# Kernel optimization log

Hardware: AMD Instinct MI355X
Metric: run time of the kernel (lower is better)

The kernel has to match this reference:

```python
import jax, jax.numpy as jnp
import numpy as np

N = 100_000   # nodes
E = 3_200_000 # edges (avg degree 32)
K = 10        # propagation hops


def setup_inputs() -> dict:
    key = jax.random.key(0)
    ks = jax.random.split(key, 9)
    x = jax.random.normal(ks[0], (N, 1), dtype=jnp.float32)
    edge_index = jax.random.randint(ks[1], (2, E), 0, N, dtype=jnp.int32)
    # MLP params (lin1: 1->32, lin2: 32->64, fc2: 64->1)
    W1 = jax.random.normal(ks[2], (1, 32), dtype=jnp.float32) * 0.5
    b1 = jnp.zeros((32,), dtype=jnp.float32)
    W2 = jax.random.normal(ks[3], (32, 64), dtype=jnp.float32) * (1.0 / np.sqrt(32))
    b2 = jnp.zeros((64,), dtype=jnp.float32)
    # GPR temp coefficients, Init='Random': uniform(-b, b), b=sqrt(3/(K+1)), L1-normalized
    bound = float(np.sqrt(3.0 / (K + 1)))
    temp = jax.random.uniform(ks[4], (K + 1,), dtype=jnp.float32,
                              minval=-bound, maxval=bound)
    temp = temp / jnp.sum(jnp.abs(temp))
    W_fc = jax.random.normal(ks[5], (64, 1), dtype=jnp.float32) * (1.0 / np.sqrt(64))
    b_fc = jnp.zeros((1,), dtype=jnp.float32)
    return {"x": x, "edge_index": edge_index, "W1": W1, "b1": b1,
            "W2": W2, "b2": b2, "temp": temp, "W_fc": W_fc, "b_fc": b_fc}


def reference(x, edge_index, W1, b1, W2, b2, temp, W_fc, b_fc):
    n = x.shape[0]
    # feature MLP
    h = jax.nn.relu(x @ W1 + b1)       # [N, 32]
    h = jax.nn.relu(h @ W2 + b2)       # [N, 64]
    # gcn_norm with self-loops, edge_weight = 1
    loops = jnp.arange(n, dtype=edge_index.dtype)
    row = jnp.concatenate([edge_index[0], loops])  # source
    col = jnp.concatenate([edge_index[1], loops])  # target (aggregation index)
    ones = jnp.ones(row.shape, dtype=h.dtype)
    deg = jax.ops.segment_sum(ones, col, num_segments=n)
    dinv = jnp.where(deg > 0, jax.lax.rsqrt(deg), 0.0)
    norm = dinv[row] * dinv[col]       # [E+N]
    # K-hop GPR propagation: hidden = sum_k temp[k] * A_hat^k h
    hidden0 = temp[0] * h

    def step(carry, gamma):
        xc, hid = carry
        msg = norm[:, None] * xc[row]                       # gather + scale
        xn = jax.ops.segment_sum(msg, col, num_segments=n)  # scatter-add
        return (xn, hid + gamma * xn), None

    (_, hidden), _ = jax.lax.scan(step, (h, hidden0), temp[1:])
    return hidden @ W_fc + b_fc        # [N, 1]
```

## Files before the change

kernel.cpp:

```cpp
#include <hip/hip_runtime.h>


#define TPB  256
#define SBSH 10
#define CAP1 34304
#define EPT  16
#define CH   (TPB * EPT)

__global__ void k_zero(int* __restrict__ bcursor, int nsb) {
    int i = blockIdx.x * blockDim.x + threadIdx.x;
    if (i < nsb) bcursor[i] = 0;
}

__global__ void k_scatter(const int* __restrict__ erow, const int* __restrict__ ecol,
                          int* __restrict__ bcursor, unsigned int* __restrict__ ebuf1,
                          int e, int nsb) {
    __shared__ int hist[128];
    __shared__ int base[128];
    int t = threadIdx.x;
    int s = blockIdx.x * CH;
    int r[EPT], c[EPT];

    if (t < 128) hist[t] = 0;
    __syncthreads();
#pragma unroll
    for (int j = 0; j < EPT; j++) {
        int i = s + j * TPB + t;
        bool ok = (i < e);
        c[j] = ok ? ecol[i] : -1;
        r[j] = ok ? erow[i] : 0;
        if (ok) atomicAdd(&hist[c[j] >> SBSH], 1);
    }
    __syncthreads();
    if (t < nsb) {
        int cc = hist[t];
        base[t] = cc ? atomicAdd(&bcursor[t], cc) : 0;
        hist[t] = 0;
    }
    __syncthreads();
#pragma unroll
    for (int j = 0; j < EPT; j++) {
        if (c[j] >= 0) {
            int b = c[j] >> SBSH;
            int pos = base[b] + atomicAdd(&hist[b], 1);
            if (pos < CAP1)
                ebuf1[(size_t)b * CAP1 + pos] =
                    ((unsigned int)r[j] << SBSH) | (unsigned int)(c[j] & ((1 << SBSH) - 1));
        }
    }
}

__global__ void __launch_bounds__(1024)
k_sub(const int* __restrict__ bcursor, const unsigned int* __restrict__ ebuf1,
      unsigned int* __restrict__ csr, int* __restrict__ rs, int* __restrict__ re,
      float* __restrict__ dinv, float* __restrict__ dinv2,
      float* __restrict__ sdeg, int n) {
    __shared__ int hist[1024];
    __shared__ int wsum[16];
    int b = blockIdx.x;
    int t = threadIdx.x;
    int lane = t & 63;
    int w = t >> 6;

    hist[t] = 0;
    __syncthreads();
    int cnt = min(bcursor[b], CAP1);
    size_t g = (size_t)b * CAP1;
    for (int j = t; j < cnt; j += 1024)
        atomicAdd(&hist[ebuf1[g + j] & 1023], 1);
    __syncthreads();

    int deg = hist[t];
    int v = deg;
#pragma unroll
    for (int o = 1; o < 64; o <<= 1) {
        int u = __shfl_up(v, o);
        if (lane >= o) v += u;
    }
    if (lane == 63) wsum[w] = v;
    __syncthreads();
    if (w == 0) {
        int sv = (lane < 16) ? wsum[lane] : 0;
#pragma unroll
        for (int o = 1; o < 16; o <<= 1) {
            int u = __shfl_up(sv, o);
            if (lane >= o) sv += u;
        }
        if (lane < 16) wsum[lane] = sv;
    }
    __syncthreads();
    int excl = v - deg + (w > 0 ? wsum[w - 1] : 0);

    int node = (b << SBSH) + t;
    if (node < n) {
        int base = (int)g + excl;
        rs[node] = base;
        re[node] = base + deg;
        float d = (float)(deg + 1);
        float di = rsqrtf(d);
        dinv[node] = di;
        dinv2[node] = di * di;
        sdeg[node] = d * di;
    }
    __syncthreads();
    hist[t] = excl;
    __syncthreads();
    for (int j = t; j < cnt; j += 1024) {
        unsigned int p = ebuf1[g + j];
        int sub = p & 1023;
        int pos = atomicAdd(&hist[sub], 1);
        csr[g + pos] = p >> SBSH;
    }
}

__global__ void k_mlp_z(const float* __restrict__ x, const float* __restrict__ W1,
                        const float* __restrict__ b1, const float* __restrict__ W2,
                        const float* __restrict__ b2, const float* __restrict__ Wfc,
                        const float* __restrict__ bfc, const float* __restrict__ temp,
                        const float* __restrict__ dinv,
                        float* __restrict__ u0, float* __restrict__ out, int n) {
    int wid = (blockIdx.x * blockDim.x + threadIdx.x) >> 6;
    int lane = threadIdx.x & 63;
    if (wid >= n) return;
    float xv = x[wid];
    float acc = b2[lane];
#pragma unroll
    for (int j = 0; j < 32; j++) {
        float h1 = fmaxf(fmaf(xv, W1[j], b1[j]), 0.f);
        acc = fmaf(h1, W2[j * 64 + lane], acc);
    }
    float h2 = fmaxf(acc, 0.f);
    float c = h2 * Wfc[lane];
#pragma unroll
    for (int o = 32; o >= 1; o >>= 1) c += __shfl_xor(c, o);
    if (lane == 0) {
        u0[wid] = dinv[wid] * c;
        out[wid] = fmaf(temp[0], c, bfc[0]);
    }
}

__global__ void k_hop(const int* __restrict__ rs, const int* __restrict__ re,
                      const unsigned int* __restrict__ csr,
                      const float* __restrict__ dinv2, const float* __restrict__ sdeg,
                      const float* __restrict__ uprev, float* __restrict__ ucur,
                      float* __restrict__ out, const float* __restrict__ temp,
                      int k, int n) {
    int tid = blockIdx.x * blockDim.x + threadIdx.x;
    int node = tid >> 3;
    int sub = tid & 7;
    if (node >= n) return;
    int s = rs[node];
    int epos = re[node];
    float sum = (sub == 0) ? uprev[node] : 0.f;
    for (int i = s + sub; i < epos; i += 8)
        sum += uprev[csr[i]];
    sum += __shfl_xor(sum, 1);
    sum += __shfl_xor(sum, 2);
    sum += __shfl_xor(sum, 4);
    if (sub == 0) {
        float u = dinv2[node] * sum;
        ucur[node] = u;
        out[node] = fmaf(temp[k] * sdeg[node], u, out[node]);
    }
}

static inline size_t align256(size_t x) { return (x + 255) & ~(size_t)255; }

extern "C" void kernel_launch(void* const* d_in, const int* in_sizes, int n_in,
                              void* d_out, int out_size, void* d_ws, size_t ws_size,
                              hipStream_t stream) {
    const float* x    = (const float*)d_in[0];
    const int*   ei   = (const int*)d_in[1];
    const float* W1   = (const float*)d_in[2];
    const float* b1   = (const float*)d_in[3];
    const float* W2   = (const float*)d_in[4];
    const float* b2   = (const float*)d_in[5];
    const float* temp = (const float*)d_in[6];
    const float* Wfc  = (const float*)d_in[7];
    const float* bfc  = (const float*)d_in[8];

    const int n = in_sizes[0];
    const int e = in_sizes[1] / 2;
    const int K = in_sizes[6] - 1;
    const int nsb = (n + (1 << SBSH) - 1) >> SBSH;

    const int* erow = ei;
    const int* ecol = ei + e;

    float* out = (float*)d_out;

    char* ws = (char*)d_ws;
    int*          bcursor = (int*)ws;          ws += align256((size_t)128 * 4);
    unsigned int* ebuf1   = (unsigned int*)ws; ws += align256((size_t)nsb * CAP1 * 4);
    unsigned int* csr     = (unsigned int*)ws; ws += align256((size_t)nsb * CAP1 * 4);
    int*          rs      = (int*)ws;          ws += align256((size_t)n * 4);
    int*          re      = (int*)ws;          ws += align256((size_t)n * 4);
    float*        dinv    = (float*)ws;        ws += align256((size_t)n * 4);
    float*        dinv2   = (float*)ws;        ws += align256((size_t)n * 4);
    float*        sdeg    = (float*)ws;        ws += align256((size_t)n * 4);
    float*        u0      = (float*)ws;        ws += align256((size_t)n * 4);
    float*        u1      = (float*)ws;        ws += align256((size_t)n * 4);

    const int gS = (e + CH - 1) / CH;
    const int gW = (n + 3) / 4;
    const int gH = (8 * n + TPB - 1) / TPB;

    k_zero<<<1, 128, 0, stream>>>(bcursor, nsb);
    k_scatter<<<gS, TPB, 0, stream>>>(erow, ecol, bcursor, ebuf1, e, nsb);
    k_sub<<<nsb, 1024, 0, stream>>>(bcursor, ebuf1, csr, rs, re, dinv, dinv2, sdeg, n);
    k_mlp_z<<<gW, 256, 0, stream>>>(x, W1, b1, W2, b2, Wfc, bfc, temp, dinv, u0, out, n);

    float* uin = u0;
    float* uout = u1;
    for (int k = 1; k <= K; k++) {
        k_hop<<<gH, TPB, 0, stream>>>(rs, re, csr, dinv2, sdeg, uin, uout, out, temp, k, n);
        float* t2 = uin; uin = uout; uout = t2;
    }
}
```

Measured before the change: 360.7 us.

## Tile source features into LDS and bin edges by source tile for hop propagation

Replaces the per-node CSR gather hop kernel with a tiled scheme. Each block owns 512 target nodes, streams the source feature vector through shared memory in 14336-element tiles, and accumulates edges with LDS atomics. The edges are re-sorted in k_sub into (half-block, source tile, sub-bin) order and packed as local src/target indices. The MLP is also moved to a one-thread-per-node kernel that runs before the scatter and zeroes the cursors, and the normalisation and initial-output work is folded into k_sub. The goal is to replace random global gathers with LDS reads. The cost is that every block reads the whole feature vector on every hop, and LDS atomic contention is added.

```diff
diff --git a/kernel.cpp b/kernel.cpp
--- a/kernel.cpp
+++ b/kernel.cpp
@@ -3,13 +3,42 @@
 
 #define TPB  256
 #define SBSH 10
-#define CAP1 34304
+#define CAP1 37376
 #define EPT  16
 #define CH   (TPB * EPT)
-
-__global__ void k_zero(int* __restrict__ bcursor, int nsb) {
+#define TILE 14336
+#define NSUB 8
+
+__global__ void k_mlp(const float* __restrict__ x, const float* __restrict__ W1,
+                      const float* __restrict__ b1, const float* __restrict__ W2,
+                      const float* __restrict__ b2, const float* __restrict__ Wfc,
+                      float* __restrict__ zarr, int* __restrict__ bcursor, int n) {
     int i = blockIdx.x * blockDim.x + threadIdx.x;
-    if (i < nsb) bcursor[i] = 0;
+    if (i < 128) bcursor[i] = 0;
+    if (i >= n) return;
+    float xv = x[i];
+    float h1[32];
+#pragma unroll
+    for (int j = 0; j < 32; j++)
+        h1[j] = fmaxf(fmaf(xv, W1[j], b1[j]), 0.f);
+    float z = 0.f;
+#pragma unroll
+    for (int fc = 0; fc < 4; fc++) {
+        float acc[16];
+#pragma unroll
+        for (int f = 0; f < 16; f++) acc[f] = b2[fc * 16 + f];
+#pragma unroll
+        for (int j = 0; j < 32; j++) {
+            float h = h1[j];
+#pragma unroll
+            for (int f = 0; f < 16; f++)
+                acc[f] = fmaf(h, W2[j * 64 + fc * 16 + f], acc[f]);
+        }
+#pragma unroll
+        for (int f = 0; f < 16; f++)
+            z = fmaf(fmaxf(acc[f], 0.f), Wfc[fc * 16 + f], z);
+    }
+    zarr[i] = z;
 }
 
 __global__ void k_scatter(const int* __restrict__ erow, const int* __restrict__ ecol,
@@ -45,126 +74,121 @@
             int pos = base[b] + atomicAdd(&hist[b], 1);
             if (pos < CAP1)
                 ebuf1[(size_t)b * CAP1 + pos] =
-                    ((unsigned int)r[j] << SBSH) | (unsigned int)(c[j] & ((1 << SBSH) - 1));
+                    ((unsigned int)r[j] << SBSH) | (unsigned int)(c[j] & 1023);
         }
     }
 }
 
 __global__ void __launch_bounds__(1024)
 k_sub(const int* __restrict__ bcursor, const unsigned int* __restrict__ ebuf1,
-      unsigned int* __restrict__ csr, int* __restrict__ rs, int* __restrict__ re,
-      float* __restrict__ dinv, float* __restrict__ dinv2,
-      float* __restrict__ sdeg, int n) {
-    __shared__ int hist[1024];
-    __shared__ int wsum[16];
+      unsigned int* __restrict__ csr, int* __restrict__ sofs,
+      float2* __restrict__ nrm, const float* __restrict__ zarr,
+      const float* __restrict__ temp, const float* __restrict__ bfc,
+      float* __restrict__ u0, float* __restrict__ out, int n, int MT) {
+    __shared__ int deg[1024];
+    __shared__ int binh[2 * 8 * NSUB];
     int b = blockIdx.x;
     int t = threadIdx.x;
-    int lane = t & 63;
-    int w = t >> 6;
-
-    hist[t] = 0;
+    int nbin = 2 * MT * NSUB;
+
+    deg[t] = 0;
+    if (t < nbin) binh[t] = 0;
     __syncthreads();
     int cnt = min(bcursor[b], CAP1);
     size_t g = (size_t)b * CAP1;
-    for (int j = t; j < cnt; j += 1024)
-        atomicAdd(&hist[ebuf1[g + j] & 1023], 1);
-    __syncthreads();
-
-    int deg = hist[t];
-    int v = deg;
-#pragma unroll
-    for (int o = 1; o < 64; o <<= 1) {
-        int u = __shfl_up(v, o);
-        if (lane >= o) v += u;
-    }
-    if (lane == 63) wsum[w] = v;
-    __syncthreads();
-    if (w == 0) {
-        int sv = (lane < 16) ? wsum[lane] : 0;
-#pragma unroll
-        for (int o = 1; o < 16; o <<= 1) {
-            int u = __shfl_up(sv, o);
-            if (lane >= o) sv += u;
-        }
-        if (lane < 16) wsum[lane] = sv;
-    }
-    __syncthreads();
-    int excl = v - deg + (w > 0 ? wsum[w - 1] : 0);
-
+    for (int j = t; j < cnt; j += 1024) {
+        unsigned int p = ebuf1[g + j];
+        int tgt = p & 1023;
+        int row = p >> SBSH;
+        int m = row / TILE;
+        int bin = ((tgt >> 9) * MT + m) * NSUB + ((row >> 11) & (NSUB - 1));
+        atomicAdd(&deg[tgt], 1);
+        atomicAdd(&binh[bin], 1);
+    }
+    __syncthreads();
+    if (t == 0) {
+        int acc = 0;
+        for (int i = 0; i < nbin; i++) { int c = binh[i]; binh[i] = acc; acc += c; }
+    }
+    __syncthreads();
+    if (t < 2 * (MT + 1)) {
+        int h = t / (MT + 1), m = t - h * (MT + 1);
+        int off;
+        if (h == 1 && m == MT) off = cnt;
+        else off = binh[(h * MT + m) * NSUB];
+        sofs[(2 * b + h) * (MT + 1) + m] = (int)g + off;
+    }
     int node = (b << SBSH) + t;
     if (node < n) {
-        int base = (int)g + excl;
-        rs[node] = base;
-        re[node] = base + deg;
-        float d = (float)(deg + 1);
+        float d = (float)(deg[t] + 1);
         float di = rsqrtf(d);
-        dinv[node] = di;
-        dinv2[node] = di * di;
-        sdeg[node] = d * di;
-    }
-    __syncthreads();
-    hist[t] = excl;
+        nrm[node] = make_float2(di * di, d * di);
+        float z = zarr[node];
+        u0[node] = di * z;
+        out[node] = fmaf(temp[0], z, bfc[0]);
+    }
     __syncthreads();
     for (int j = t; j < cnt; j += 1024) {
         unsigned int p = ebuf1[g + j];
-        int sub = p & 1023;
-        int pos = atomicAdd(&hist[sub], 1);
-        csr[g + pos] = p >> SBSH;
-    }
-}
-
-__global__ void k_mlp_z(const float* __restrict__ x, const float* __restrict__ W1,
-                        const float* __restrict__ b1, const float* __restrict__ W2,
-                        const float* __restrict__ b2, const float* __restrict__ Wfc,
-                        const float* __restrict__ bfc, const float* __restrict__ temp,
-                        const float* __restrict__ dinv,
-                        float* __restrict__ u0, float* __restrict__ out, int n) {
-    int wid = (blockIdx.x * blockDim.x + threadIdx.x) >> 6;
-    int lane = threadIdx.x & 63;
-    if (wid >= n) return;
-    float xv = x[wid];
-    float acc = b2[lane];
-#pragma unroll
-    for (int j = 0; j < 32; j++) {
-        float h1 = fmaxf(fmaf(xv, W1[j], b1[j]), 0.f);
-        acc = fmaf(h1, W2[j * 64 + lane], acc);
-    }
-    float h2 = fmaxf(acc, 0.f);
-    float c = h2 * Wfc[lane];
-#pragma unroll
-    for (int o = 32; o >= 1; o >>= 1) c += __shfl_xor(c, o);
-    if (lane == 0) {
-        u0[wid] = dinv[wid] * c;
-        out[wid] = fmaf(temp[0], c, bfc[0]);
-    }
-}
-
-__global__ void k_hop(const int* __restrict__ rs, const int* __restrict__ re,
-                      const unsigned int* __restrict__ csr,
-                      const float* __restrict__ dinv2, const float* __restrict__ sdeg,
-                      const float* __restrict__ uprev, float* __restrict__ ucur,
-                      float* __restrict__ out, const float* __restrict__ temp,
-                      int k, int n) {
-    int tid = blockIdx.x * blockDim.x + threadIdx.x;
-    int node = tid >> 3;
-    int sub = tid & 7;
-    if (node >= n) return;
-    int s = rs[node];
-    int epos = re[node];
-    float sum = (sub == 0) ? uprev[node] : 0.f;
-    for (int i = s + sub; i < epos; i += 8)
-        sum += uprev[csr[i]];
-    sum += __shfl_xor(sum, 1);
-    sum += __shfl_xor(sum, 2);
-    sum += __shfl_xor(sum, 4);
-    if (sub == 0) {
-        float u = dinv2[node] * sum;
-        ucur[node] = u;
-        out[node] = fmaf(temp[k] * sdeg[node], u, out[node]);
-    }
-}
-
-static inline size_t align256(size_t x) { return (x + 255) & ~(size_t)255; }
+        int tgt = p & 1023;
+        int row = p >> SBSH;
+        int m = row / TILE;
+        int bin = ((tgt >> 9) * MT + m) * NSUB + ((row >> 11) & (NSUB - 1));
+        int pos = atomicAdd(&binh[bin], 1);
+        int srcl = row - m * TILE;
+        csr[g + pos] = ((unsigned int)srcl << 9) | (unsigned int)(tgt & 511);
+    }
+}
+
+__global__ void __launch_bounds__(512)
+k_hop(const int* __restrict__ sofs, const unsigned int* __restrict__ csr,
+      const float2* __restrict__ nrm, const float* __restrict__ uprev,
+      float* __restrict__ ucur, float* __restrict__ out,
+      const float* __restrict__ temp, int k, int K, int n, int MT) {
+    __shared__ float tile[TILE];
+    __shared__ float acc[512];
+    int hb = blockIdx.x;
+    int t = threadIdx.x;
+    const float4* u4 = (const float4*)uprev;
+    float4* t4 = (float4*)tile;
+    float4 rv[TILE / 2048];
+
+#pragma unroll
+    for (int q = 0; q < TILE / 2048; q++)
+        rv[q] = u4[q * 512 + t];
+    acc[t] = 0.f;
+
+    int sb = hb * (MT + 1);
+    for (int m = 0; m < MT; m++) {
+        __syncthreads();
+#pragma unroll
+        for (int q = 0; q < TILE / 2048; q++)
+            t4[q * 512 + t] = rv[q];
+        __syncthreads();
+        if (m + 1 < MT) {
+            size_t b4 = (size_t)(m + 1) * (TILE / 4);
+#pragma unroll
+            for (int q = 0; q < TILE / 2048; q++)
+                rv[q] = u4[b4 + q * 512 + t];
+        }
+        int j0 = sofs[sb + m], j1 = sofs[sb + m + 1];
+        for (int j = j0 + t; j < j1; j += 512) {
+            unsigned int p = csr[j];
+            atomicAdd(&acc[p & 511], tile[p >> 9]);
+        }
+    }
+    __syncthreads();
+    int node = (hb << 9) + t;
+    if (node < n) {
+        float2 nv = nrm[node];
+        float sum = acc[t] + uprev[node];
+        float u = nv.x * sum;
+        if (k < K) ucur[node] = u;
+        out[node] = fmaf(temp[k] * nv.y, u, out[node]);
+    }
+}
+
+static inline size_t align256(size_t v) { return (v + 255) & ~(size_t)255; }
 
 extern "C" void kernel_launch(void* const* d_in, const int* in_sizes, int n_in,
                               void* d_out, int out_size, void* d_ws, size_t ws_size,
@@ -183,37 +207,39 @@
     const int e = in_sizes[1] / 2;
     const int K = in_sizes[6] - 1;
     const int nsb = (n + (1 << SBSH) - 1) >> SBSH;
+    const int MT  = (n + TILE - 1) / TILE;
+    const int nhb = 2 * nsb;
 
     const int* erow = ei;
     const int* ecol = ei + e;
 
     float* out = (float*)d_out;
+
+    const size_t upad = (size_t)MT * TILE + 256;
 
     char* ws = (char*)d_ws;
     int*          bcursor = (int*)ws;          ws += align256((size_t)128 * 4);
     unsigned int* ebuf1   = (unsigned int*)ws; ws += align256((size_t)nsb * CAP1 * 4);
     unsigned int* csr     = (unsigned int*)ws; ws += align256((size_t)nsb * CAP1 * 4);
-    int*          rs      = (int*)ws;          ws += align256((size_t)n * 4);
-    int*          re      = (int*)ws;          ws += align256((size_t)n * 4);
-    float*        dinv    = (float*)ws;        ws += align256((size_t)n * 4);
-    float*        dinv2   = (float*)ws;        ws += align256((size_t)n * 4);
-    float*        sdeg    = (float*)ws;        ws += align256((size_t)n * 4);
-    float*        u0      = (float*)ws;        ws += align256((size_t)n * 4);
-    float*        u1      = (float*)ws;        ws += align256((size_t)n * 4);
-
+    int*          sofs    = (int*)ws;          ws += align256((size_t)nhb * (MT + 1) * 4);
+    float2*       nrm     = (float2*)ws;       ws += align256((size_t)n * 8);
+    float*        zarr    = (float*)ws;        ws += align256((size_t)n * 4);
+    float*        u0      = (float*)ws;        ws += align256(upad * 4);
+    float*        u1      = (float*)ws;        ws += align256(upad * 4);
+
+    const int gM = (n + TPB - 1) / TPB;
     const int gS = (e + CH - 1) / CH;
-    const int gW = (n + 3) / 4;
-    const int gH = (8 * n + TPB - 1) / TPB;
-
-    k_zero<<<1, 128, 0, stream>>>(bcursor, nsb);
+
+    k_mlp<<<gM, TPB, 0, stream>>>(x, W1, b1, W2, b2, Wfc, zarr, bcursor, n);
     k_scatter<<<gS, TPB, 0, stream>>>(erow, ecol, bcursor, ebuf1, e, nsb);
-    k_sub<<<nsb, 1024, 0, stream>>>(bcursor, ebuf1, csr, rs, re, dinv, dinv2, sdeg, n);
-    k_mlp_z<<<gW, 256, 0, stream>>>(x, W1, b1, W2, b2, Wfc, bfc, temp, dinv, u0, out, n);
+    k_sub<<<nsb, 1024, 0, stream>>>(bcursor, ebuf1, csr, sofs, nrm,
+                                    zarr, temp, bfc, u0, out, n, MT);
 
     float* uin = u0;
     float* uout = u1;
     for (int k = 1; k <= K; k++) {
-        k_hop<<<gH, TPB, 0, stream>>>(rs, re, csr, dinv2, sdeg, uin, uout, out, temp, k, n);
+        k_hop<<<nhb, 512, 0, stream>>>(sofs, csr, nrm, uin, uout, out,
+                                       temp, k, K, n, MT);
         float* t2 = uin; uin = uout; uout = t2;
     }
 }
```

Result: slower. 654.2 us (+81.4%).
